# Kernel optimization log

Measured on AMD Instinct MI355X. Metric: run time of the kernel, lower is better.

The kernel has to match this reference:

```python
import jax, jax.numpy as jnp
import numpy as np

D_MODEL = 1024
NUM_HEADS = 16

def setup_inputs() -> dict:
    key = jax.random.key(0)
    ks = jax.random.split(key, 5)
    std = np.sqrt(2.0 / (D_MODEL + D_MODEL))
    def w(k):
        # trunc_normal approx: normal clipped to +-3 std
        v = jax.random.truncated_normal(k, -3.0, 3.0, (D_MODEL, D_MODEL), dtype=jnp.float32) * std
        return v
    return {
        "x": jax.random.normal(ks[0], (2, 2048, D_MODEL), dtype=jnp.float32),
        "w_q": w(ks[1]),
        "w_k": w(ks[2]),
        "w_v": w(ks[3]),
        "w_o": w(ks[4]),
    }

def reference(x, w_q, w_k, w_v, w_o):
    B, S, D = x.shape
    H = NUM_HEADS
    dk = D // H
    # Linear: y = x @ W^T  (weight is [d_out, d_in])
    def proj(w):
        y = jnp.einsum('bsd,ed->bse', x, w)
        return y.reshape(B, S, H, dk).transpose(0, 2, 1, 3)  # [B,H,S,dk]
    q, k, v = proj(w_q), proj(w_k), proj(w_v)
    scale = 1.0 / jnp.sqrt(jnp.float32(dk))
    scores = jnp.einsum('bhqd,bhkd->bhqk', q, k) * scale  # [B,H,S,S]
    causal = jnp.tril(jnp.ones((S, S), dtype=bool))
    scores = jnp.where(causal, scores, -jnp.inf)
    attn = jax.nn.softmax(scores, axis=-1)
    out = jnp.einsum('bhqk,bhkd->bhqd', attn, v)  # [B,H,S,dk]
    out = out.transpose(0, 2, 1, 3).reshape(B, S, D)
    return jnp.einsum('bsd,ed->bse', out, w_o)
```

## Files before the change

kernel.cpp:

```cpp
#include <hip/hip_runtime.h>
#include <hip/hip_bf16.h>
#include <stdint.h>

#define S_LEN 2048
#define DM    1024
#define NH    16
#define DK    64
#define NBATCH 2

typedef __attribute__((ext_vector_type(8))) short bf8_t;
typedef __attribute__((ext_vector_type(4))) short s4_t;
typedef __attribute__((ext_vector_type(4))) float f4_t;

using bf16 = __hip_bfloat16;

#define NEG_BIG (-1.0e30f)
#define SCALE2  (0.125f * 1.44269504088896f)

static __device__ __forceinline__ f4_t mfma16(bf8_t a, bf8_t b, f4_t c) {
    return __builtin_amdgcn_mfma_f32_16x16x32_bf16(a, b, c, 0, 0, 0);
}

static __device__ __forceinline__ short f2b(float f) {
    __hip_bfloat16 h = __float2bfloat16(f);
    return *reinterpret_cast<short*>(&h);
}

static __device__ __forceinline__ void g2l16(const bf16* g, bf16* l) {
#if __has_builtin(__builtin_amdgcn_global_load_lds)
    __builtin_amdgcn_global_load_lds(
        (const __attribute__((address_space(1))) void*)g,
        (__attribute__((address_space(3))) void*)l, 16, 0, 0);
#else
    *(bf8_t*)l = *(const bf8_t*)g;
#endif
}

__global__ __launch_bounds__(256)
void cvt_all(const float* __restrict__ x,  const float* __restrict__ wq,
             const float* __restrict__ wk, const float* __restrict__ wv,
             const float* __restrict__ wo, bf16* __restrict__ ob) {
    const size_t SEG = 1u << 20;
    size_t i = ((size_t)blockIdx.x * 256 + threadIdx.x) * 8;
    const float* src;
    if      (i < 4 * SEG) src = x  + i;
    else if (i < 5 * SEG) src = wq + (i - 4 * SEG);
    else if (i < 6 * SEG) src = wk + (i - 5 * SEG);
    else if (i < 7 * SEG) src = wv + (i - 6 * SEG);
    else                  src = wo + (i - 7 * SEG);
    float4 f0 = *(const float4*)(src);
    float4 f1 = *(const float4*)(src + 4);
    bf8_t v;
    v[0]=f2b(f0.x); v[1]=f2b(f0.y); v[2]=f2b(f0.z); v[3]=f2b(f0.w);
    v[4]=f2b(f1.x); v[5]=f2b(f1.y); v[6]=f2b(f1.z); v[7]=f2b(f1.w);
    *(bf8_t*)(ob + i) = v;
}

#define GEMM_B_MAINLOOP(Aptr, Bptr)                                          \
    __shared__ bf16 As[128][32];                                             \
    __shared__ bf16 Bs[128][32];                                             \
    const int tid  = threadIdx.x;                                            \
    const int lane = tid & 63;                                               \
    const int w    = tid >> 6;                                               \
    const int wr   = w >> 1, wc = w & 1;                                     \
    const int lhi  = lane >> 4, llo = lane & 15;                             \
    const int bm   = blockIdx.x * 128;                                       \
    const int bn   = blockIdx.y * 128;                                       \
    const int r0c  = tid >> 2;                           \
    const int c0c  = (tid & 3) << 3;                     \
    const int r1c  = (256 + tid) >> 2;                                       \
    f4_t acc[4][4] = {};                                                     \
    for (int k0 = 0; k0 < 1024; k0 += 32) {                                  \
        __syncthreads();                                                     \
        g2l16(Aptr + (size_t)(bm + r0c) * 1024 + k0 + c0c,                   \
              &As[0][0] + (size_t)tid * 8);                                  \
        g2l16(Aptr + (size_t)(bm + r1c) * 1024 + k0 + c0c,                   \
              &As[0][0] + (size_t)(256 + tid) * 8);                          \
        g2l16(Bptr + (size_t)(bn + r0c) * 1024 + k0 + c0c,                   \
              &Bs[0][0] + (size_t)tid * 8);                                  \
        g2l16(Bptr + (size_t)(bn + r1c) * 1024 + k0 + c0c,                   \
              &Bs[0][0] + (size_t)(256 + tid) * 8);                          \
        asm volatile("s_waitcnt vmcnt(0)" ::: "memory");                     \
        __syncthreads();                                                     \
        bf8_t af[4], bfr[4];                                                 \
        _Pragma("unroll")                                                    \
        for (int i = 0; i < 4; ++i) {                                        \
            af[i]  = *(const bf8_t*)(&As[wr * 64 + i * 16 + llo][lhi * 8]);  \
            bfr[i] = *(const bf8_t*)(&Bs[wc * 64 + i * 16 + llo][lhi * 8]);  \
        }                                                                    \
        _Pragma("unroll")                                                    \
        for (int mi = 0; mi < 4; ++mi)                                       \
            _Pragma("unroll")                                                \
            for (int ni = 0; ni < 4; ++ni)                                   \
                acc[mi][ni] = mfma16(af[mi], bfr[ni], acc[mi][ni]);          \
    }

__global__ __launch_bounds__(256)
void gemm_qkv_b(const bf16* __restrict__ xb,
                const bf16* __restrict__ wqb, const bf16* __restrict__ wkb,
                const bf16* __restrict__ wvb,
                bf16* __restrict__ qws, bf16* __restrict__ kws,
                bf16* __restrict__ vtws) {
    const int z = blockIdx.z;
    const bf16* Wb = (z == 0) ? wqb : (z == 1) ? wkb : wvb;
    GEMM_B_MAINLOOP(xb, Wb)

    if (z < 2) {
        bf16* C = z ? kws : qws;
        const float sc = z ? 1.0f : SCALE2;
        #pragma unroll
        for (int mi = 0; mi < 4; ++mi)
            #pragma unroll
            for (int ni = 0; ni < 4; ++ni)
                #pragma unroll
                for (int r = 0; r < 4; ++r) {
                    int m = bm + wr * 64 + mi * 16 + lhi * 4 + r;
                    int n = bn + wc * 64 + ni * 16 + llo;
                    int b = m >> 11, s = m & (S_LEN - 1);
                    int h = n >> 6,  d = n & (DK - 1);
                    C[(((size_t)(b * NH + h) * S_LEN) + s) * DK + d] =
                        __float2bfloat16(acc[mi][ni][r] * sc);
                }
    } else {
        #pragma unroll
        for (int mi = 0; mi < 4; ++mi)
            #pragma unroll
            for (int ni = 0; ni < 4; ++ni) {
                int m0 = bm + wr * 64 + mi * 16 + lhi * 4;
                int n  = bn + wc * 64 + ni * 16 + llo;
                int b = m0 >> 11, s0 = m0 & (S_LEN - 1);
                int h = n >> 6,   d  = n & (DK - 1);
                s4_t pk;
                #pragma unroll
                for (int r = 0; r < 4; ++r) pk[r] = f2b(acc[mi][ni][r]);
                *(s4_t*)&vtws[(((size_t)(b * NH + h) * DK) + d) * S_LEN + s0] = pk;
            }
    }
}

__global__ __launch_bounds__(256)
void gemm_o_b(const bf16* __restrict__ A, const bf16* __restrict__ Wb,
              float* __restrict__ C) {
    __shared__ bf16 As[128][32];
    __shared__ bf16 Bs[64][32];
    const int tid  = threadIdx.x;
    const int lane = tid & 63;
    const int w    = tid >> 6;
    const int wr   = w >> 1, wc = w & 1;
    const int lhi  = lane >> 4, llo = lane & 15;
    const int bm   = blockIdx.x * 128;
    const int bn   = blockIdx.y * 64;
    const int r0c  = tid >> 2;
    const int c0c  = (tid & 3) << 3;
    const int r1c  = (256 + tid) >> 2;
    f4_t acc[4][2] = {};
    for (int k0 = 0; k0 < 1024; k0 += 32) {
        __syncthreads();
        g2l16(A + (size_t)(bm + r0c) * 1024 + k0 + c0c,
              &As[0][0] + (size_t)tid * 8);
        g2l16(A + (size_t)(bm + r1c) * 1024 + k0 + c0c,
              &As[0][0] + (size_t)(256 + tid) * 8);
        g2l16(Wb + (size_t)(bn + r0c) * 1024 + k0 + c0c,
              &Bs[0][0] + (size_t)tid * 8);
        asm volatile("s_waitcnt vmcnt(0)" ::: "memory");
        __syncthreads();
        bf8_t af[4], bfr[2];
        #pragma unroll
        for (int i = 0; i < 4; ++i)
            af[i] = *(const bf8_t*)(&As[wr * 64 + i * 16 + llo][lhi * 8]);
        #pragma unroll
        for (int i = 0; i < 2; ++i)
            bfr[i] = *(const bf8_t*)(&Bs[wc * 32 + i * 16 + llo][lhi * 8]);
        #pragma unroll
        for (int mi = 0; mi < 4; ++mi)
            #pragma unroll
            for (int ni = 0; ni < 2; ++ni)
                acc[mi][ni] = mfma16(af[mi], bfr[ni], acc[mi][ni]);
    }
    #pragma unroll
    for (int mi = 0; mi < 4; ++mi)
        #pragma unroll
        for (int ni = 0; ni < 2; ++ni)
            #pragma unroll
            for (int r = 0; r < 4; ++r) {
                int m = bm + wr * 64 + mi * 16 + lhi * 4 + r;
                int n = bn + wc * 32 + ni * 16 + llo;
                C[(size_t)m * DM + n] = acc[mi][ni][r];
            }
}

__global__ __launch_bounds__(256)
void gemm_qkv_f32(const float* __restrict__ x,
                  const float* __restrict__ wqp, const float* __restrict__ wkp,
                  const float* __restrict__ wvp,
                  bf16* __restrict__ qws, bf16* __restrict__ kws,
                  bf16* __restrict__ vtws) {
    constexpr int K = DM;
    constexpr int BM = 128, BK = 32, LDT = BK + 8;
    const int z = blockIdx.z;
    const float* W = (z == 0) ? wqp : (z == 1) ? wkp : wvp;
    __shared__ bf16 As[BM][LDT];
    __shared__ bf16 Bs[BM][LDT];
    const int tid  = threadIdx.x;
    const int lane = tid & 63;
    const int w    = tid >> 6;
    const int wr   = w >> 1, wc = w & 1;
    const int lhi  = lane >> 4, llo = lane & 15;
    const int bm   = blockIdx.x * BM;
    const int bn   = blockIdx.y * BM;
    f4_t acc[4][4] = {};
    for (int k0 = 0; k0 < K; k0 += BK) {
        __syncthreads();
        #pragma unroll
        for (int t = 0; t < 2; ++t) {
            int c   = t * 256 + tid;
            int row = c >> 2;
            int col = (c & 3) << 3;
            {
                const float* s0 = x + (size_t)(bm + row) * K + k0 + col;
                float4 f0 = *(const float4*)(s0);
                float4 f1 = *(const float4*)(s0 + 4);
                bf8_t a8;
                a8[0]=f2b(f0.x); a8[1]=f2b(f0.y); a8[2]=f2b(f0.z); a8[3]=f2b(f0.w);
                a8[4]=f2b(f1.x); a8[5]=f2b(f1.y); a8[6]=f2b(f1.z); a8[7]=f2b(f1.w);
                *(bf8_t*)(&As[row][col]) = a8;
            }
            {
                const float* s0 = W + (size_t)(bn + row) * K + k0 + col;
                float4 f0 = *(const float4*)(s0);
                float4 f1 = *(const float4*)(s0 + 4);
                bf8_t b8;
                b8[0]=f2b(f0.x); b8[1]=f2b(f0.y); b8[2]=f2b(f0.z); b8[3]=f2b(f0.w);
                b8[4]=f2b(f1.x); b8[5]=f2b(f1.y); b8[6]=f2b(f1.z); b8[7]=f2b(f1.w);
                *(bf8_t*)(&Bs[row][col]) = b8;
            }
        }
        __syncthreads();
        bf8_t af[4], bfr[4];
        #pragma unroll
        for (int i = 0; i < 4; ++i) {
            af[i]  = *(const bf8_t*)(&As[wr * 64 + i * 16 + llo][lhi * 8]);
            bfr[i] = *(const bf8_t*)(&Bs[wc * 64 + i * 16 + llo][lhi * 8]);
        }
        #pragma unroll
        for (int mi = 0; mi < 4; ++mi)
            #pragma unroll
            for (int ni = 0; ni < 4; ++ni)
                acc[mi][ni] = mfma16(af[mi], bfr[ni], acc[mi][ni]);
    }
    if (z < 2) {
        bf16* C = z ? kws : qws;
        const float sc = z ? 1.0f : SCALE2;
        #pragma unroll
        for (int mi = 0; mi < 4; ++mi)
            #pragma unroll
            for (int ni = 0; ni < 4; ++ni)
                #pragma unroll
                for (int r = 0; r < 4; ++r) {
                    int m = bm + wr * 64 + mi * 16 + lhi * 4 + r;
                    int n = bn + wc * 64 + ni * 16 + llo;
                    int b = m >> 11, s = m & (S_LEN - 1);
                    int h = n >> 6,  d = n & (DK - 1);
                    C[(((size_t)(b * NH + h) * S_LEN) + s) * DK + d] =
                        __float2bfloat16(acc[mi][ni][r] * sc);
                }
    } else {
        #pragma unroll
        for (int mi = 0; mi < 4; ++mi)
            #pragma unroll
            for (int ni = 0; ni < 4; ++ni) {
                int m0 = bm + wr * 64 + mi * 16 + lhi * 4;
                int n  = bn + wc * 64 + ni * 16 + llo;
                int b = m0 >> 11, s0 = m0 & (S_LEN - 1);
                int h = n >> 6,   d  = n & (DK - 1);
                s4_t pk;
                #pragma unroll
                for (int r = 0; r < 4; ++r) pk[r] = f2b(acc[mi][ni][r]);
                *(s4_t*)&vtws[(((size_t)(b * NH + h) * DK) + d) * S_LEN + s0] = pk;
            }
    }
}

__global__ __launch_bounds__(256)
void gemm_o_f32(const bf16* __restrict__ A, const float* __restrict__ W,
                float* __restrict__ C) {
    constexpr int N = DM;
    constexpr int K = DM;
    constexpr int BM = 128, BN = 64, BK = 32, LDT = BK + 8;
    __shared__ bf16 As[BM][LDT];
    __shared__ bf16 Bs[BN][LDT];
    const int tid  = threadIdx.x;
    const int lane = tid & 63;
    const int w    = tid >> 6;
    const int wr   = w >> 1, wc = w & 1;
    const int lhi  = lane >> 4, llo = lane & 15;
    const int bm   = blockIdx.x * BM;
    const int bn   = blockIdx.y * BN;
    f4_t acc[4][2] = {};
    for (int k0 = 0; k0 < K; k0 += BK) {
        __syncthreads();
        #pragma unroll
        for (int t = 0; t < 2; ++t) {
            int c   = t * 256 + tid;
            int row = c >> 2;
            int col = (c & 3) << 3;
            *(bf8_t*)(&As[row][col]) =
                *(const bf8_t*)(A + (size_t)(bm + row) * K + k0 + col);
        }
        {
            int row = tid >> 2;
            int col = (tid & 3) << 3;
            const float* s0 = W + (size_t)(bn + row) * K + k0 + col;
            float4 f0 = *(const float4*)(s0);
            float4 f1 = *(const float4*)(s0 + 4);
            bf8_t b8;
            b8[0]=f2b(f0.x); b8[1]=f2b(f0.y); b8[2]=f2b(f0.z); b8[3]=f2b(f0.w);
            b8[4]=f2b(f1.x); b8[5]=f2b(f1.y); b8[6]=f2b(f1.z); b8[7]=f2b(f1.w);
            *(bf8_t*)(&Bs[row][col]) = b8;
        }
        __syncthreads();
        bf8_t af[4], bfr[2];
        #pragma unroll
        for (int i = 0; i < 4; ++i)
            af[i] = *(const bf8_t*)(&As[wr * 64 + i * 16 + llo][lhi * 8]);
        #pragma unroll
        for (int i = 0; i < 2; ++i)
            bfr[i] = *(const bf8_t*)(&Bs[wc * 32 + i * 16 + llo][lhi * 8]);
        #pragma unroll
        for (int mi = 0; mi < 4; ++mi)
            #pragma unroll
            for (int ni = 0; ni < 2; ++ni)
                acc[mi][ni] = mfma16(af[mi], bfr[ni], acc[mi][ni]);
    }
    #pragma unroll
    for (int mi = 0; mi < 4; ++mi)
        #pragma unroll
        for (int ni = 0; ni < 2; ++ni)
            #pragma unroll
            for (int r = 0; r < 4; ++r) {
                int m = bm + wr * 64 + mi * 16 + lhi * 4 + r;
                int n = bn + wc * 32 + ni * 16 + llo;
                C[(size_t)m * N + n] = acc[mi][ni][r];
            }
}

__global__ __launch_bounds__(512, 4)
void attn_fwd(const bf16* __restrict__ Q, const bf16* __restrict__ K,
              const bf16* __restrict__ Vt, bf16* __restrict__ AO) {
    __shared__ bf16 Ks[2][2][64][64];
    __shared__ bf16 Vs[2][2][64][64];

    const int bh = blockIdx.x;
    const int qt = 31 - (int)blockIdx.y;
    const int q0 = qt * 64;
    const int nt = qt + 1;
    const int S  = (nt + 1) >> 1;

    const bf16* Qh = Q  + (size_t)bh * S_LEN * DK;
    const bf16* Kh = K  + (size_t)bh * S_LEN * DK;
    const bf16* Vh = Vt + (size_t)bh * DK * S_LEN;

    const int tid  = threadIdx.x;
    const int lane = tid & 63;
    const int w    = tid >> 6;
    const int g    = w >> 2;
    const int qsub = w & 3;
    const int lhi  = lane >> 4, llo = lane & 15;
    const int qw   = q0 + qsub * 16;
    const int sw   = llo & 7;

    const int srow = tid >> 3;
    const int schk = (tid & 7) ^ (srow & 7);
    const int gk = (((srow >> 2) & 3) << 3) | (((srow >> 4) & 1) << 2)
                 | (srow & 3) | ((srow >> 5) << 5);

#define STAGE(t, gg, b)                                                       \
    do {                                                                      \
        const int kv_ = (t) * 64;                                             \
        g2l16(Kh + (size_t)(kv_ + gk) * DK + schk * 8,                        \
              &Ks[gg][b][0][0] + (size_t)tid * 8);                            \
        g2l16(Vh + (size_t)srow * S_LEN + kv_ + schk * 8,                     \
              &Vs[gg][b][0][0] + (size_t)tid * 8);                            \
    } while (0)

    const bf16* qrow = Qh + (size_t)(qw + llo) * DK;
    const bf8_t qf0 = *(const bf8_t*)(qrow + lhi * 8);
    const bf8_t qf1 = *(const bf8_t*)(qrow + 32 + lhi * 8);

    bf8_t ones;
    #pragma unroll
    for (int j = 0; j < 8; ++j) ones[j] = (short)0x3F80;

    STAGE(0, 0, 0);
    if (1 < nt) STAGE(1, 1, 0);
    asm volatile("s_waitcnt vmcnt(0)" ::: "memory");
    __syncthreads();

    f4_t o[4] = {};
    float lr[4] = {0.f, 0.f, 0.f, 0.f};
    float mr = NEG_BIG;

    for (int s = 0; s < S; ++s) {
        const int tg  = 2 * s + g;
        const int cur = s & 1;
        const int tn0 = 2 * (s + 1);
        if (tn0 < nt)     STAGE(tn0,     0, cur ^ 1);
        if (tn0 + 1 < nt) STAGE(tn0 + 1, 1, cur ^ 1);

        const int kv0 = tg * 64;
        if (tg < nt && kv0 <= qw + 15) {
            f4_t sc[4] = {};
            __builtin_amdgcn_s_setprio(1);
            #pragma unroll
            for (int nf = 0; nf < 4; ++nf) {
                const int R = nf * 16 + llo;
                bf8_t k0f = *(const bf8_t*)&Ks[g][cur][R][(lhi ^ sw) * 8];
                bf8_t k1f = *(const bf8_t*)&Ks[g][cur][R][((4 + lhi) ^ sw) * 8];
                sc[nf] = mfma16(k0f, qf0, sc[nf]);
                sc[nf] = mfma16(k1f, qf1, sc[nf]);
            }
            __builtin_amdgcn_s_setprio(0);

            if (kv0 + 63 > qw) {
                #pragma unroll
                for (int nf = 0; nf < 4; ++nf)
                    #pragma unroll
                    for (int r = 0; r < 4; ++r)
                        if (kv0 + lhi * 8 + ((nf & 1) << 2) + r + ((nf >> 1) << 5)
                            > qw + llo)
                            sc[nf][r] = NEG_BIG;
            }

            float pm = sc[0][0];
            #pragma unroll
            for (int nf = 0; nf < 4; ++nf)
                #pragma unroll
                for (int r = 0; r < 4; ++r) pm = fmaxf(pm, sc[nf][r]);
            pm = fmaxf(pm, __shfl_xor(pm, 16));
            pm = fmaxf(pm, __shfl_xor(pm, 32));

            if (__any(pm > mr + 8.0f)) {
                float mn = fmaxf(mr, pm);
                float alpha = exp2f(mr - mn);
                mr = mn;
                float ao[4];
                #pragma unroll
                for (int r = 0; r < 4; ++r) ao[r] = __shfl(alpha, lhi * 4 + r);
                #pragma unroll
                for (int df = 0; df < 4; ++df)
                    #pragma unroll
                    for (int r = 0; r < 4; ++r) o[df][r] *= ao[r];
                #pragma unroll
                for (int r = 0; r < 4; ++r) lr[r] *= ao[r];
            }

            bf8_t pa0, pa1;
            #pragma unroll
            for (int r = 0; r < 4; ++r) {
                pa0[r]     = f2b(exp2f(sc[0][r] - mr));
                pa0[4 + r] = f2b(exp2f(sc[1][r] - mr));
                pa1[r]     = f2b(exp2f(sc[2][r] - mr));
                pa1[4 + r] = f2b(exp2f(sc[3][r] - mr));
            }

            f4_t rsacc = {};
            rsacc = mfma16(pa0, ones, rsacc);
            rsacc = mfma16(pa1, ones, rsacc);

            __builtin_amdgcn_s_setprio(1);
            #pragma unroll
            for (int df = 0; df < 4; ++df) {
                const int R = df * 16 + llo;
                bf8_t vb0 = *(const bf8_t*)&Vs[g][cur][R][(lhi ^ sw) * 8];
                bf8_t vb1 = *(const bf8_t*)&Vs[g][cur][R][((4 + lhi) ^ sw) * 8];
                o[df] = mfma16(pa0, vb0, o[df]);
                o[df] = mfma16(pa1, vb1, o[df]);
            }
            __builtin_amdgcn_s_setprio(0);

            #pragma unroll
            for (int r = 0; r < 4; ++r) lr[r] += rsacc[r];
        }

        asm volatile("s_waitcnt vmcnt(0)" ::: "memory");
        __syncthreads();
    }
#undef STAGE

    float mo[4];
    #pragma unroll
    for (int r = 0; r < 4; ++r) mo[r] = __shfl(mr, lhi * 4 + r);

    float* xch = (float*)&Ks[0][0][0][0];
    if (g == 1) {
        float* p = xch + ((size_t)(qsub * 64 + lane)) * 24;
        #pragma unroll
        for (int df = 0; df < 4; ++df)
            #pragma unroll
            for (int r = 0; r < 4; ++r) p[df * 4 + r] = o[df][r];
        #pragma unroll
        for (int r = 0; r < 4; ++r) { p[16 + r] = lr[r]; p[20 + r] = mo[r]; }
    }
    __syncthreads();
    if (g == 0) {
        const float* p = xch + ((size_t)(qsub * 64 + lane)) * 24;
        const int b = bh >> 4, h = bh & (NH - 1);
        #pragma unroll
        for (int r = 0; r < 4; ++r) {
            float m1 = p[20 + r];
            float M  = fmaxf(mo[r], m1);
            float a0 = exp2f(mo[r] - M);
            float a1 = exp2f(m1 - M);
            float l  = lr[r] * a0 + p[16 + r] * a1;
            float inv = 1.0f / l;
            int q = qw + lhi * 4 + r;
            bf16* orow = AO + ((size_t)(b * S_LEN + q) * DM) + h * DK;
            #pragma unroll
            for (int df = 0; df < 4; ++df) {
                float v = o[df][r] * a0 + p[df * 4 + r] * a1;
                orow[df * 16 + llo] = __float2bfloat16(v * inv);
            }
        }
    }
}

extern "C" void kernel_launch(void* const* d_in, const int* in_sizes, int n_in,
                              void* d_out, int out_size, void* d_ws, size_t ws_size,
                              hipStream_t stream) {
    const float* x  = (const float*)d_in[0];
    const float* wq = (const float*)d_in[1];
    const float* wk = (const float*)d_in[2];
    const float* wv = (const float*)d_in[3];
    const float* wo = (const float*)d_in[4];
    float* out = (float*)d_out;

    const size_t SEG   = 1u << 20;
    const size_t elems = 4 * SEG;
    const size_t need_fast = (8 * SEG + 3 * elems) * sizeof(bf16);

    dim3 blk(256);

    if (ws_size >= need_fast) {
        bf16* ob   = (bf16*)d_ws;
        bf16* xb   = ob;
        bf16* wqb  = ob + 4 * SEG;
        bf16* wkb  = ob + 5 * SEG;
        bf16* wvb  = ob + 6 * SEG;
        bf16* wob  = ob + 7 * SEG;
        bf16* qws  = ob + 8 * SEG;
        bf16* kws  = qws + elems;
        bf16* vtws = kws + elems;
        bf16* aws  = xb;

        cvt_all<<<4096, blk, 0, stream>>>(x, wq, wk, wv, wo, ob);
        gemm_qkv_b<<<dim3(32, 8, 3), blk, 0, stream>>>(xb, wqb, wkb, wvb,
                                                       qws, kws, vtws);
        attn_fwd<<<dim3(NBATCH * NH, 32), dim3(512), 0, stream>>>(qws, kws, vtws, aws);
        gemm_o_b<<<dim3(32, 16), blk, 0, stream>>>(aws, wob, out);
    } else {
        if (ws_size < elems * 4 * sizeof(bf16)) return;
        bf16* qws  = (bf16*)d_ws;
        bf16* kws  = qws + elems;
        bf16* vtws = kws + elems;
        bf16* aws  = vtws + elems;

        gemm_qkv_f32<<<dim3(32, 8, 3), blk, 0, stream>>>(x, wq, wk, wv,
                                                         qws, kws, vtws);
        attn_fwd<<<dim3(NBATCH * NH, 32), dim3(512), 0, stream>>>(qws, kws, vtws, aws);
        gemm_o_f32<<<dim3(32, 16), blk, 0, stream>>>(aws, wo, out);
    }
}
```

Measured before the change: 103.6 us.

## Halve attention KV tile to 32 and shrink LDS to raise occupancy

The attention kernel now stages 32-key K/V tiles instead of 64, cutting shared memory from 64KB to 32KB, and raises the launch bound to 8 blocks per CU. K and V loads are split across the two halves of the block, and the V layout is rearranged so that one MFMA per output fragment covers the 32 keys. The aim is higher occupancy and less wasted causal work at tile granularity. In exchange the loop runs twice as many iterations, with more barriers, more online-softmax rescale checks, and tighter register limits that may cause spills.

```diff
diff --git a/kernel.cpp b/kernel.cpp
--- a/kernel.cpp
+++ b/kernel.cpp
@@ -344,17 +344,18 @@
             }
 }
 
-__global__ __launch_bounds__(512, 4)
+__global__ __launch_bounds__(512, 8)
 void attn_fwd(const bf16* __restrict__ Q, const bf16* __restrict__ K,
               const bf16* __restrict__ Vt, bf16* __restrict__ AO) {
-    __shared__ bf16 Ks[2][2][64][64];
-    __shared__ bf16 Vs[2][2][64][64];
+    __shared__ __align__(16) unsigned char smem[32768];
+    bf16 (*Ks)[2][32][64] = reinterpret_cast<bf16(*)[2][32][64]>(smem);
+    bf16 (*Vs)[2][32][64] = reinterpret_cast<bf16(*)[2][32][64]>(smem + 16384);
 
     const int bh = blockIdx.x;
     const int qt = 31 - (int)blockIdx.y;
     const int q0 = qt * 64;
-    const int nt = qt + 1;
-    const int S  = (nt + 1) >> 1;
+    const int nt = 2 * (qt + 1);
+    const int S  = qt + 1;
 
     const bf16* Qh = Q  + (size_t)bh * S_LEN * DK;
     const bf16* Kh = K  + (size_t)bh * S_LEN * DK;
@@ -367,20 +368,24 @@
     const int qsub = w & 3;
     const int lhi  = lane >> 4, llo = lane & 15;
     const int qw   = q0 + qsub * 16;
-    const int sw   = llo & 7;
-
-    const int srow = tid >> 3;
+    const int sw7  = llo & 7;
+
+    const int srow = (tid & 255) >> 3;
     const int schk = (tid & 7) ^ (srow & 7);
-    const int gk = (((srow >> 2) & 3) << 3) | (((srow >> 4) & 1) << 2)
-                 | (srow & 3) | ((srow >> 5) << 5);
+    const int gk = (((srow >> 2) & 3) << 3) | (((srow >> 4) & 1) << 2) | (srow & 3);
+    const int vl  = (tid & 7) ^ (srow & 7);
+    const int vd  = ((vl >> 2) << 5) + srow;
+    const int vkc = (vl & 3) << 3;
 
 #define STAGE(t, gg, b)                                                       \
     do {                                                                      \
-        const int kv_ = (t) * 64;                                             \
-        g2l16(Kh + (size_t)(kv_ + gk) * DK + schk * 8,                        \
-              &Ks[gg][b][0][0] + (size_t)tid * 8);                            \
-        g2l16(Vh + (size_t)srow * S_LEN + kv_ + schk * 8,                     \
-              &Vs[gg][b][0][0] + (size_t)tid * 8);                            \
+        const int kv_ = (t) * 32;                                             \
+        if (tid < 256)                                                        \
+            g2l16(Kh + (size_t)(kv_ + gk) * DK + schk * 8,                    \
+                  &Ks[gg][b][0][0] + (size_t)tid * 8);                        \
+        else                                                                  \
+            g2l16(Vh + (size_t)vd * S_LEN + kv_ + vkc,                        \
+                  &Vs[gg][b][0][0] + (size_t)(tid - 256) * 8);                \
     } while (0)
 
     const bf16* qrow = Qh + (size_t)(qw + llo) * DK;
@@ -392,7 +397,7 @@
     for (int j = 0; j < 8; ++j) ones[j] = (short)0x3F80;
 
     STAGE(0, 0, 0);
-    if (1 < nt) STAGE(1, 1, 0);
+    STAGE(1, 1, 0);
     asm volatile("s_waitcnt vmcnt(0)" ::: "memory");
     __syncthreads();
 
@@ -404,38 +409,37 @@
         const int tg  = 2 * s + g;
         const int cur = s & 1;
         const int tn0 = 2 * (s + 1);
-        if (tn0 < nt)     STAGE(tn0,     0, cur ^ 1);
-        if (tn0 + 1 < nt) STAGE(tn0 + 1, 1, cur ^ 1);
-
-        const int kv0 = tg * 64;
-        if (tg < nt && kv0 <= qw + 15) {
-            f4_t sc[4] = {};
+        if (tn0 < nt) {
+            STAGE(tn0,     0, cur ^ 1);
+            STAGE(tn0 + 1, 1, cur ^ 1);
+        }
+
+        const int kv0 = tg * 32;
+        if (kv0 <= qw + 15) {
+            f4_t s0 = {}, s1 = {};
             __builtin_amdgcn_s_setprio(1);
-            #pragma unroll
-            for (int nf = 0; nf < 4; ++nf) {
-                const int R = nf * 16 + llo;
-                bf8_t k0f = *(const bf8_t*)&Ks[g][cur][R][(lhi ^ sw) * 8];
-                bf8_t k1f = *(const bf8_t*)&Ks[g][cur][R][((4 + lhi) ^ sw) * 8];
-                sc[nf] = mfma16(k0f, qf0, sc[nf]);
-                sc[nf] = mfma16(k1f, qf1, sc[nf]);
+            {
+                bf8_t k00 = *(const bf8_t*)&Ks[g][cur][llo][(lhi ^ sw7) * 8];
+                bf8_t k01 = *(const bf8_t*)&Ks[g][cur][llo][((4 + lhi) ^ sw7) * 8];
+                s0 = mfma16(k00, qf0, s0);
+                s0 = mfma16(k01, qf1, s0);
+                bf8_t k10 = *(const bf8_t*)&Ks[g][cur][16 + llo][(lhi ^ sw7) * 8];
+                bf8_t k11 = *(const bf8_t*)&Ks[g][cur][16 + llo][((4 + lhi) ^ sw7) * 8];
+                s1 = mfma16(k10, qf0, s1);
+                s1 = mfma16(k11, qf1, s1);
             }
             __builtin_amdgcn_s_setprio(0);
 
-            if (kv0 + 63 > qw) {
-                #pragma unroll
-                for (int nf = 0; nf < 4; ++nf)
-                    #pragma unroll
-                    for (int r = 0; r < 4; ++r)
-                        if (kv0 + lhi * 8 + ((nf & 1) << 2) + r + ((nf >> 1) << 5)
-                            > qw + llo)
-                            sc[nf][r] = NEG_BIG;
-            }
-
-            float pm = sc[0][0];
-            #pragma unroll
-            for (int nf = 0; nf < 4; ++nf)
-                #pragma unroll
-                for (int r = 0; r < 4; ++r) pm = fmaxf(pm, sc[nf][r]);
+            if (kv0 + 31 > qw) {
+                #pragma unroll
+                for (int r = 0; r < 4; ++r) {
+                    if (kv0 + lhi * 8 + r     > qw + llo) s0[r] = NEG_BIG;
+                    if (kv0 + lhi * 8 + 4 + r > qw + llo) s1[r] = NEG_BIG;
+                }
+            }
+
+            float pm = fmaxf(fmaxf(fmaxf(s0[0], s0[1]), fmaxf(s0[2], s0[3])),
+                             fmaxf(fmaxf(s1[0], s1[1]), fmaxf(s1[2], s1[3])));
             pm = fmaxf(pm, __shfl_xor(pm, 16));
             pm = fmaxf(pm, __shfl_xor(pm, 32));
 
@@ -454,27 +458,23 @@
                 for (int r = 0; r < 4; ++r) lr[r] *= ao[r];
             }
 
-            bf8_t pa0, pa1;
+            bf8_t pa;
             #pragma unroll
             for (int r = 0; r < 4; ++r) {
-                pa0[r]     = f2b(exp2f(sc[0][r] - mr));
-                pa0[4 + r] = f2b(exp2f(sc[1][r] - mr));
-                pa1[r]     = f2b(exp2f(sc[2][r] - mr));
-                pa1[4 + r] = f2b(exp2f(sc[3][r] - mr));
+                pa[r]     = f2b(exp2f(s0[r] - mr));
+                pa[4 + r] = f2b(exp2f(s1[r] - mr));
             }
 
             f4_t rsacc = {};
-            rsacc = mfma16(pa0, ones, rsacc);
-            rsacc = mfma16(pa1, ones, rsacc);
+            rsacc = mfma16(pa, ones, rsacc);
 
             __builtin_amdgcn_s_setprio(1);
             #pragma unroll
             for (int df = 0; df < 4; ++df) {
-                const int R = df * 16 + llo;
-                bf8_t vb0 = *(const bf8_t*)&Vs[g][cur][R][(lhi ^ sw) * 8];
-                bf8_t vb1 = *(const bf8_t*)&Vs[g][cur][R][((4 + lhi) ^ sw) * 8];
-                o[df] = mfma16(pa0, vb0, o[df]);
-                o[df] = mfma16(pa1, vb1, o[df]);
+                const int vr = ((df & 1) << 4) + llo;
+                const int lp = (((df >> 1) << 2) + lhi) ^ sw7;
+                bf8_t vb = *(const bf8_t*)&Vs[g][cur][vr][lp * 8];
+                o[df] = mfma16(pa, vb, o[df]);
             }
             __builtin_amdgcn_s_setprio(0);
 
@@ -491,7 +491,7 @@
     #pragma unroll
     for (int r = 0; r < 4; ++r) mo[r] = __shfl(mr, lhi * 4 + r);
 
-    float* xch = (float*)&Ks[0][0][0][0];
+    float* xch = (float*)smem;
     if (g == 1) {
         float* p = xch + ((size_t)(qsub * 64 + lane)) * 24;
         #pragma unroll
```

After: 107.5 us. 3.7% more time.

## Double-buffer LDS tiles in bf16 GEMM main loops to overlap loads with MFMA

Applied to the files above, without the earlier changes.

Both the QKV and output-projection bf16 GEMMs now keep two shared-memory tile buffers. The next K-slice is issued with direct global-to-LDS loads before the MFMAs run on the current slice. This hides global-memory latency behind compute and removes one barrier per iteration. In exchange, shared-memory use doubles, which may lower occupancy, and the wait at the end of each iteration still serializes on all loads.

```diff
diff --git a/kernel.cpp b/kernel.cpp
--- a/kernel.cpp
+++ b/kernel.cpp
@@ -57,8 +57,8 @@
 }
 
 #define GEMM_B_MAINLOOP(Aptr, Bptr)                                          \
-    __shared__ bf16 As[128][32];                                             \
-    __shared__ bf16 Bs[128][32];                                             \
+    __shared__ bf16 As[2][128][32];                                          \
+    __shared__ bf16 Bs[2][128][32];                                          \
     const int tid  = threadIdx.x;                                            \
     const int lane = tid & 63;                                               \
     const int w    = tid >> 6;                                               \
@@ -70,29 +70,43 @@
     const int c0c  = (tid & 3) << 3;                     \
     const int r1c  = (256 + tid) >> 2;                                       \
     f4_t acc[4][4] = {};                                                     \
-    for (int k0 = 0; k0 < 1024; k0 += 32) {                                  \
-        __syncthreads();                                                     \
-        g2l16(Aptr + (size_t)(bm + r0c) * 1024 + k0 + c0c,                   \
-              &As[0][0] + (size_t)tid * 8);                                  \
-        g2l16(Aptr + (size_t)(bm + r1c) * 1024 + k0 + c0c,                   \
-              &As[0][0] + (size_t)(256 + tid) * 8);                          \
-        g2l16(Bptr + (size_t)(bn + r0c) * 1024 + k0 + c0c,                   \
-              &Bs[0][0] + (size_t)tid * 8);                                  \
-        g2l16(Bptr + (size_t)(bn + r1c) * 1024 + k0 + c0c,                   \
-              &Bs[0][0] + (size_t)(256 + tid) * 8);                          \
-        asm volatile("s_waitcnt vmcnt(0)" ::: "memory");                     \
-        __syncthreads();                                                     \
+                                      \
+    g2l16(Aptr + (size_t)(bm + r0c) * 1024 + c0c,                            \
+          &As[0][0][0] + (size_t)tid * 8);                                   \
+    g2l16(Aptr + (size_t)(bm + r1c) * 1024 + c0c,                            \
+          &As[0][0][0] + (size_t)(256 + tid) * 8);                           \
+    g2l16(Bptr + (size_t)(bn + r0c) * 1024 + c0c,                            \
+          &Bs[0][0][0] + (size_t)tid * 8);                                   \
+    g2l16(Bptr + (size_t)(bn + r1c) * 1024 + c0c,                            \
+          &Bs[0][0][0] + (size_t)(256 + tid) * 8);                           \
+    asm volatile("s_waitcnt vmcnt(0)" ::: "memory");                         \
+    __syncthreads();                                                         \
+    for (int t = 0; t < 32; ++t) {                                           \
+        const int cur = t & 1;                                               \
+        if (t + 1 < 32) {       \
+            const int k1 = (t + 1) * 32;                                     \
+            g2l16(Aptr + (size_t)(bm + r0c) * 1024 + k1 + c0c,               \
+                  &As[cur ^ 1][0][0] + (size_t)tid * 8);                     \
+            g2l16(Aptr + (size_t)(bm + r1c) * 1024 + k1 + c0c,               \
+                  &As[cur ^ 1][0][0] + (size_t)(256 + tid) * 8);             \
+            g2l16(Bptr + (size_t)(bn + r0c) * 1024 + k1 + c0c,               \
+                  &Bs[cur ^ 1][0][0] + (size_t)tid * 8);                     \
+            g2l16(Bptr + (size_t)(bn + r1c) * 1024 + k1 + c0c,               \
+                  &Bs[cur ^ 1][0][0] + (size_t)(256 + tid) * 8);             \
+        }                                                                    \
         bf8_t af[4], bfr[4];                                                 \
         _Pragma("unroll")                                                    \
         for (int i = 0; i < 4; ++i) {                                        \
-            af[i]  = *(const bf8_t*)(&As[wr * 64 + i * 16 + llo][lhi * 8]);  \
-            bfr[i] = *(const bf8_t*)(&Bs[wc * 64 + i * 16 + llo][lhi * 8]);  \
+            af[i]  = *(const bf8_t*)(&As[cur][wr*64 + i*16 + llo][lhi*8]);   \
+            bfr[i] = *(const bf8_t*)(&Bs[cur][wc*64 + i*16 + llo][lhi*8]);   \
         }                                                                    \
         _Pragma("unroll")                                                    \
         for (int mi = 0; mi < 4; ++mi)                                       \
             _Pragma("unroll")                                                \
             for (int ni = 0; ni < 4; ++ni)                                   \
                 acc[mi][ni] = mfma16(af[mi], bfr[ni], acc[mi][ni]);          \
+        asm volatile("s_waitcnt vmcnt(0)" ::: "memory");                     \
+        __syncthreads();                                                     \
     }
 
 __global__ __launch_bounds__(256)
@@ -141,8 +155,8 @@
 __global__ __launch_bounds__(256)
 void gemm_o_b(const bf16* __restrict__ A, const bf16* __restrict__ Wb,
               float* __restrict__ C) {
-    __shared__ bf16 As[128][32];
-    __shared__ bf16 Bs[64][32];
+    __shared__ bf16 As[2][128][32];
+    __shared__ bf16 Bs[2][64][32];
     const int tid  = threadIdx.x;
     const int lane = tid & 63;
     const int w    = tid >> 6;
@@ -154,28 +168,37 @@
     const int c0c  = (tid & 3) << 3;
     const int r1c  = (256 + tid) >> 2;
     f4_t acc[4][2] = {};
-    for (int k0 = 0; k0 < 1024; k0 += 32) {
-        __syncthreads();
-        g2l16(A + (size_t)(bm + r0c) * 1024 + k0 + c0c,
-              &As[0][0] + (size_t)tid * 8);
-        g2l16(A + (size_t)(bm + r1c) * 1024 + k0 + c0c,
-              &As[0][0] + (size_t)(256 + tid) * 8);
-        g2l16(Wb + (size_t)(bn + r0c) * 1024 + k0 + c0c,
-              &Bs[0][0] + (size_t)tid * 8);
+    g2l16(A + (size_t)(bm + r0c) * 1024 + c0c, &As[0][0][0] + (size_t)tid * 8);
+    g2l16(A + (size_t)(bm + r1c) * 1024 + c0c,
+          &As[0][0][0] + (size_t)(256 + tid) * 8);
+    g2l16(Wb + (size_t)(bn + r0c) * 1024 + c0c, &Bs[0][0][0] + (size_t)tid * 8);
+    asm volatile("s_waitcnt vmcnt(0)" ::: "memory");
+    __syncthreads();
+    for (int t = 0; t < 32; ++t) {
+        const int cur = t & 1;
+        if (t + 1 < 32) {
+            const int k1 = (t + 1) * 32;
+            g2l16(A + (size_t)(bm + r0c) * 1024 + k1 + c0c,
+                  &As[cur ^ 1][0][0] + (size_t)tid * 8);
+            g2l16(A + (size_t)(bm + r1c) * 1024 + k1 + c0c,
+                  &As[cur ^ 1][0][0] + (size_t)(256 + tid) * 8);
+            g2l16(Wb + (size_t)(bn + r0c) * 1024 + k1 + c0c,
+                  &Bs[cur ^ 1][0][0] + (size_t)tid * 8);
+        }
+        bf8_t af[4], bfr[2];
+        #pragma unroll
+        for (int i = 0; i < 4; ++i)
+            af[i] = *(const bf8_t*)(&As[cur][wr * 64 + i * 16 + llo][lhi * 8]);
+        #pragma unroll
+        for (int i = 0; i < 2; ++i)
+            bfr[i] = *(const bf8_t*)(&Bs[cur][wc * 32 + i * 16 + llo][lhi * 8]);
+        #pragma unroll
+        for (int mi = 0; mi < 4; ++mi)
+            #pragma unroll
+            for (int ni = 0; ni < 2; ++ni)
+                acc[mi][ni] = mfma16(af[mi], bfr[ni], acc[mi][ni]);
         asm volatile("s_waitcnt vmcnt(0)" ::: "memory");
         __syncthreads();
-        bf8_t af[4], bfr[2];
-        #pragma unroll
-        for (int i = 0; i < 4; ++i)
-            af[i] = *(const bf8_t*)(&As[wr * 64 + i * 16 + llo][lhi * 8]);
-        #pragma unroll
-        for (int i = 0; i < 2; ++i)
-            bfr[i] = *(const bf8_t*)(&Bs[wc * 32 + i * 16 + llo][lhi * 8]);
-        #pragma unroll
-        for (int mi = 0; mi < 4; ++mi)
-            #pragma unroll
-            for (int ni = 0; ni < 2; ++ni)
-                acc[mi][ni] = mfma16(af[mi], bfr[ni], acc[mi][ni]);
     }
     #pragma unroll
     for (int mi = 0; mi < 4; ++mi)
```

Measured after the change: 110.5 us. +6.7%, slower.
